# Kernel optimization log

Hardware: AMD Instinct MI355X
Metric: run time of the kernel (lower is better)

The kernel has to match this reference:

```python
import jax, jax.numpy as jnp
import numpy as np

# MSEObserver config: bit=4, symmetric=False, ch_axis=-1
QMIN, QMAX = 0, 15          # asymmetric int4: [0, 2^4 - 1]
NUM = 100                   # range-grid resolution
EPS = np.float32(np.finfo(np.float32).eps)


def setup_inputs() -> dict:
    key = jax.random.key(0)
    x_orig = jax.random.normal(key, (1024, 4096), dtype=jnp.float32)
    return {"x_orig": x_orig}


def _search_2d(x):
    # per-tensor (ch_axis == -1) 2D grid search over (range, zero_point)
    x_min = jnp.min(x)
    x_max = jnp.max(x)
    xrange = x_max - x_min
    qrange = float(QMAX - QMIN)
    zps = jnp.arange(QMIN, QMAX + 1, dtype=jnp.float32)  # [Z] candidate zp shifts

    def step(carry, i):
        best_score, best_min, best_max = carry
        tmp_max = xrange / NUM * i           # tmp_min == 0
        tmp_delta = tmp_max / qrange
        new_min = jnp.maximum(-zps * tmp_delta, x_min)           # [Z]
        new_max = jnp.minimum(tmp_max - zps * tmp_delta, x_max)  # [Z]
        # calculate_qparams (asymmetric)
        min_neg = jnp.minimum(new_min, 0.0)
        max_pos = jnp.maximum(new_max, 0.0)
        scale = jnp.maximum((max_pos - min_neg) / qrange, EPS)   # [Z]
        zp = jnp.clip(QMIN - jnp.round(min_neg / scale), QMIN, QMAX)  # [Z]
        s = scale[:, None, None]
        z = zp[:, None, None]
        # fake_quantize_per_tensor_affine, vectorized over Z candidates
        xq = (jnp.clip(jnp.round(x[None] / s) + z, QMIN, QMAX) - z) * s  # [Z,T,D]
        score = jnp.mean(jnp.square(xq - x[None]), axis=(1, 2))  # [Z], lp_loss p=2
        j = jnp.argmin(score)
        sc = score[j]
        better = sc < best_score
        best_min = jnp.where(better, new_min[j], best_min)
        best_max = jnp.where(better, new_max[j], best_max)
        best_score = jnp.minimum(best_score, sc)
        return (best_score, best_min, best_max), None

    init = (jnp.float32(1e10), x_min, x_max)
    iis = jnp.arange(1, NUM + 1, dtype=jnp.float32)
    (best_score, best_min, best_max), _ = jax.lax.scan(step, init, iis)
    return best_min, best_max


def reference(x_orig) -> jnp.ndarray:
    # randn input => one_side_dist == 'no', symmetric == False -> perform_2D_search
    x = x_orig.astype(jnp.float32)
    best_min, best_max = _search_2d(x)
    # buffer update: min_val = min(+inf, best_min), max_val = max(-inf, best_max)
    return jnp.stack([best_min, best_max])
```

## Files before the change

kernel.cpp:

```cpp
#include <hip/hip_runtime.h>
#include <math.h>

#define NUM_I 100
#define NZ    16
#define NCAND (NUM_I * NZ)
#define NBL   4096
#define G2    256
#define BLK   1024
#define SLICE 16384
#define BPT   (NBL / BLK)
#define F32_EPS 1.1920928955078125e-07f
#define AGENT __HIP_MEMORY_SCOPE_AGENT

struct WSL {
    unsigned* ctrs;
    double*   score;
    float*    pmin; float* pmax;
    float4*   params; float2* ranges; float* mm;
    double*   scoreFB;
    size_t    small_needed;
};

__host__ __device__ static inline WSL make_ws(char* w0) {
    WSL L; char* w = w0;
    L.ctrs   = (unsigned*)w; w += 64;
    L.score  = (double*)w;   w += sizeof(double) * NCAND;
    L.pmin   = (float*)w;    w += sizeof(float) * G2;
    L.pmax   = (float*)w;    w += sizeof(float) * G2;
    L.params = (float4*)w;   w += sizeof(float4) * NCAND;
    L.ranges = (float2*)w;   w += sizeof(float2) * NCAND;
    L.mm     = (float*)w;    w += sizeof(float) * 4;
    size_t head = (size_t)(w - w0);
    L.small_needed = (head + 15) & ~(size_t)15;
    L.scoreFB = L.score;
    return L;
}

static __device__ __forceinline__ float rfl_f(float v) {
    return __int_as_float(__builtin_amdgcn_readfirstlane(__float_as_int(v)));
}
static __device__ __forceinline__ double agent_load_f64(const double* p) {
    return __hip_atomic_load(p, __ATOMIC_RELAXED, AGENT);
}
static __device__ __forceinline__ int bin_loc(float v, float lo, float invw) {
    int b = (int)floorf((v - lo) * invw);
    return min(max(b, 0), NBL - 1);
}
static __device__ __forceinline__ void gbar(unsigned* ctr, int nblk) {
    __syncthreads();
    if (threadIdx.x == 0) {
        __hip_atomic_fetch_add(ctr, 1u, __ATOMIC_ACQ_REL, AGENT);
        while (__hip_atomic_load(ctr, __ATOMIC_RELAXED, AGENT) < (unsigned)nblk)
            __builtin_amdgcn_s_sleep(8);
        (void)__hip_atomic_load(ctr, __ATOMIC_ACQUIRE, AGENT);
    }
    __syncthreads();
}

__global__ __launch_bounds__(BLK, 4) void k_fused(const float* __restrict__ x, int n4,
                                                  char* wsbase, float* __restrict__ out) {
    WSL L = make_ws(wsbase);
    __shared__ __align__(16) float ssort[SLICE];
    __shared__ unsigned Cb[NBL];
    __shared__ double   S1p[NBL];
    __shared__ double   dpart[BLK];
    __shared__ unsigned upart[BLK];
    __shared__ double   stot[1];
    __shared__ float    sxm[2];
    __shared__ int      islast;
    const int tid = threadIdx.x, blk = blockIdx.x;
    const float4* x4 = (const float4*)x;
    const int per4 = (n4 + G2 - 1) / G2;
    const int beg4 = blk * per4, end4 = min(beg4 + per4, n4);
    const int len = (end4 > beg4) ? (end4 - beg4) * 4 : 0;

    {
        int gtid = blk * BLK + tid;
        if (gtid < NCAND) L.score[gtid] = 0.0;
        float* rmin = (float*)dpart; float* rmax = rmin + BLK;
        float lmin = 3.0e38f, lmax = -3.0e38f;
        for (int i = beg4 + tid; i < end4; i += BLK) {
            float4 v = x4[i];
            lmin = fminf(lmin, fminf(fminf(v.x, v.y), fminf(v.z, v.w)));
            lmax = fmaxf(lmax, fmaxf(fmaxf(v.x, v.y), fmaxf(v.z, v.w)));
        }
        rmin[tid] = lmin; rmax[tid] = lmax;
        __syncthreads();
        for (int s = BLK / 2; s > 0; s >>= 1) {
            if (tid < s) {
                rmin[tid] = fminf(rmin[tid], rmin[tid + s]);
                rmax[tid] = fmaxf(rmax[tid], rmax[tid + s]);
            }
            __syncthreads();
        }
        if (tid == 0) { L.pmin[blk] = rmin[0]; L.pmax[blk] = rmax[0]; }
    }
    gbar(&L.ctrs[0], G2);

    {
        float* rmin = (float*)dpart; float* rmax = rmin + BLK;
        float lmin = (tid < G2) ? L.pmin[tid] : 3.0e38f;
        float lmax = (tid < G2) ? L.pmax[tid] : -3.0e38f;
        rmin[tid] = lmin; rmax[tid] = lmax;
        __syncthreads();
        for (int s = BLK / 2; s > 0; s >>= 1) {
            if (tid < s) {
                rmin[tid] = fminf(rmin[tid], rmin[tid + s]);
                rmax[tid] = fmaxf(rmax[tid], rmax[tid + s]);
            }
            __syncthreads();
        }
        if (tid == 0) { sxm[0] = rmin[0]; sxm[1] = rmax[0]; }
        __syncthreads();
    }
    const float x_min = sxm[0], x_max = sxm[1];
    const float rangef = x_max - x_min;
    const float lo = x_min;
    const float invw = (rangef > 0.0f) ? ((float)NBL / rangef) : 0.0f;

    if (len > 0) {
        for (int b = tid; b < NBL; b += BLK) Cb[b] = 0u;
        __syncthreads();
        for (int i = beg4 + tid; i < end4; i += BLK) {
            float4 v = x4[i];
            atomicAdd(&Cb[bin_loc(v.x, lo, invw)], 1u);
            atomicAdd(&Cb[bin_loc(v.y, lo, invw)], 1u);
            atomicAdd(&Cb[bin_loc(v.z, lo, invw)], 1u);
            atomicAdd(&Cb[bin_loc(v.w, lo, invw)], 1u);
        }
        __syncthreads();
        unsigned cl[BPT]; unsigned ps = 0;
        #pragma unroll
        for (int k = 0; k < BPT; k++) { cl[k] = Cb[tid * BPT + k]; ps += cl[k]; }
        upart[tid] = ps;
        __syncthreads();
        for (int off = 1; off < BLK; off <<= 1) {
            unsigned v = (tid >= off) ? upart[tid - off] : 0u;
            __syncthreads();
            upart[tid] += v;
            __syncthreads();
        }
        unsigned run = upart[tid] - ps;
        #pragma unroll
        for (int k = 0; k < BPT; k++) { Cb[tid * BPT + k] = run; run += cl[k]; }
        __syncthreads();
        for (int i = beg4 + tid; i < end4; i += BLK) {
            float4 v = x4[i];
            unsigned p;
            p = atomicAdd(&Cb[bin_loc(v.x, lo, invw)], 1u); ssort[p] = v.x;
            p = atomicAdd(&Cb[bin_loc(v.y, lo, invw)], 1u); ssort[p] = v.y;
            p = atomicAdd(&Cb[bin_loc(v.z, lo, invw)], 1u); ssort[p] = v.z;
            p = atomicAdd(&Cb[bin_loc(v.w, lo, invw)], 1u); ssort[p] = v.w;
        }
        __syncthreads();
        for (int k = 0; k < BPT; k++) {
            int b = tid + k * BLK;
            unsigned st = (b == 0) ? 0u : Cb[b - 1], en = Cb[b];
            double s1 = 0.0;
            for (unsigned i = st; i < en; i++) s1 += (double)ssort[i];
            S1p[b] = s1;
        }
        __syncthreads();
        double l1[BPT];
        double a1 = 0.0;
        #pragma unroll
        for (int k = 0; k < BPT; k++) { l1[k] = S1p[tid * BPT + k]; a1 += l1[k]; }
        dpart[tid] = a1;
        __syncthreads();
        for (int off = 1; off < BLK; off <<= 1) {
            double v1 = (tid >= off) ? dpart[tid - off] : 0.0;
            __syncthreads();
            dpart[tid] += v1;
            __syncthreads();
        }
        double b1 = dpart[tid] - a1;
        #pragma unroll
        for (int k = 0; k < BPT; k++) {
            int b = tid * BPT + k;
            S1p[b] = b1; b1 += l1[k];
        }
        if (tid == BLK - 1) stot[0] = dpart[BLK - 1];
        __syncthreads();

        const double totS1 = stot[0];
        for (int q = 0; q < (NCAND + BLK - 1) / BLK; q++) {
            int cand = q * BLK + ((tid + blk) & (BLK - 1));
            if (cand >= NCAND) continue;
            int zi; double sd;
            {
#pragma clang fp contract(off)
                float step = rangef / 100.0f;
                int ii = cand >> 4, z = cand & 15;
                float fi = (float)(ii + 1);
                float tmp_max   = step * fi;
                float tmp_delta = tmp_max / 15.0f;
                float t = (float)z * tmp_delta;
                float new_min = fmaxf(-t, x_min);
                float new_max = fminf(tmp_max - t, x_max);
                float min_neg = fminf(new_min, 0.0f);
                float max_pos = fmaxf(new_max, 0.0f);
                float scale = fmaxf((max_pos - min_neg) / 15.0f, F32_EPS);
                float zp = 0.0f - rintf(min_neg / scale);
                zp = fminf(fmaxf(zp, 0.0f), 15.0f);
                zi = (int)zp; sd = (double)scale;
            }
            double prevC = 0.0, prev1 = 0.0, sc = 0.0;
            for (int j = 0; j <= 15; j++) {
                double Cc, C1;
                if (j < 15) {
                    double td = ((double)(j - zi) + 0.5) * sd;
                    float tf = (float)td;
                    int bf = bin_loc(tf, lo, invw);
                    unsigned st = (bf == 0) ? 0u : Cb[bf - 1], en = Cb[bf];
                    unsigned cnt = 0; double s1 = 0.0;
                    unsigned i = st;
                    for (; i < en && (i & 3u); i++) {
                        float v = ssort[i];
                        if (v < tf) { cnt++; s1 += (double)v; }
                    }
                    for (; i + 4u <= en; i += 4u) {
                        float4 v4 = *reinterpret_cast<const float4*>(&ssort[i]);
                        float m0 = (v4.x < tf) ? v4.x : 0.0f;
                        float m1 = (v4.y < tf) ? v4.y : 0.0f;
                        float m2 = (v4.z < tf) ? v4.z : 0.0f;
                        float m3 = (v4.w < tf) ? v4.w : 0.0f;
                        cnt += (v4.x < tf); cnt += (v4.y < tf);
                        cnt += (v4.z < tf); cnt += (v4.w < tf);
                        s1 += (double)((m0 + m1) + (m2 + m3));
                    }
                    for (; i < en; i++) {
                        float v = ssort[i];
                        if (v < tf) { cnt++; s1 += (double)v; }
                    }
                    Cc = (double)st + (double)cnt;
                    C1 = S1p[bf] + s1;
                } else {
                    Cc = (double)len; C1 = totS1;
                }
                double ms = (double)(j - zi) * sd;
                sc += ms * (ms * (Cc - prevC) - 2.0 * (C1 - prev1));
                prevC = Cc; prev1 = C1;
            }
            atomicAdd(&L.score[cand], sc);
        }
    }

    __syncthreads();
    if (tid == 0) {
        __threadfence();
        unsigned old = atomicAdd(&L.ctrs[1], 1u);
        islast = (old == gridDim.x - 1) ? 1 : 0;
    }
    __syncthreads();
    if (!islast) return;
    __threadfence();

    double* bsc = dpart;
    int*    bix = (int*)upart;
    double best = 1.0e300; int bidx = 0x7fffffff;
    for (int c = tid; c < NCAND; c += BLK) {
        double sc = agent_load_f64(&L.score[c]);
        if (sc < best) { best = sc; bidx = c; }
    }
    bsc[tid] = best; bix[tid] = bidx;
    __syncthreads();
    for (int s = BLK / 2; s > 0; s >>= 1) {
        if (tid < s) {
            double so = bsc[tid + s]; int io = bix[tid + s];
            if (so < bsc[tid] || (so == bsc[tid] && io < bix[tid])) { bsc[tid] = so; bix[tid] = io; }
        }
        __syncthreads();
    }
    if (tid == 0) {
        float bmin = x_min, bmax = x_max;
        if (bix[0] != 0x7fffffff) {
#pragma clang fp contract(off)
            int cand = bix[0];
            float step = rangef / 100.0f;
            int ii = cand >> 4, z = cand & 15;
            float fi = (float)(ii + 1);
            float tmp_max   = step * fi;
            float tmp_delta = tmp_max / 15.0f;
            float t = (float)z * tmp_delta;
            bmin = fmaxf(-t, x_min);
            bmax = fminf(tmp_max - t, x_max);
        }
        out[0] = bmin; out[1] = bmax;
    }
}

__global__ __launch_bounds__(256) void k_params_fb(const float* __restrict__ x, int n4,
                                                   float4* __restrict__ params,
                                                   float2* __restrict__ ranges,
                                                   double* __restrict__ score,
                                                   float* __restrict__ mm) {
#pragma clang fp contract(off)
    __shared__ float smin[256], smax[256];
    const float4* x4 = (const float4*)x;
    float lmin = 3.0e38f, lmax = -3.0e38f;
    for (int i = threadIdx.x; i < n4; i += 256) {
        float4 v = x4[i];
        lmin = fminf(lmin, fminf(fminf(v.x, v.y), fminf(v.z, v.w)));
        lmax = fmaxf(lmax, fmaxf(fmaxf(v.x, v.y), fmaxf(v.z, v.w)));
    }
    smin[threadIdx.x] = lmin; smax[threadIdx.x] = lmax;
    __syncthreads();
    for (int s = 128; s > 0; s >>= 1) {
        if (threadIdx.x < s) {
            smin[threadIdx.x] = fminf(smin[threadIdx.x], smin[threadIdx.x + s]);
            smax[threadIdx.x] = fmaxf(smax[threadIdx.x], smax[threadIdx.x + s]);
        }
        __syncthreads();
    }
    float x_min = smin[0], x_max = smax[0];
    if (threadIdx.x == 0) { mm[0] = x_min; mm[1] = x_max; }
    float xrange = x_max - x_min;
    float step = xrange / 100.0f;
    for (int c = threadIdx.x; c < NCAND; c += 256) {
        int ii = c >> 4;
        int z  = c & 15;
        float fi = (float)(ii + 1);
        float tmp_max   = step * fi;
        float tmp_delta = tmp_max / 15.0f;
        float t = (float)z * tmp_delta;
        float new_min = fmaxf(-t, x_min);
        float new_max = fminf(tmp_max - t, x_max);
        float min_neg = fminf(new_min, 0.0f);
        float max_pos = fmaxf(new_max, 0.0f);
        float scale = fmaxf((max_pos - min_neg) / 15.0f, F32_EPS);
        float zp = 0.0f - rintf(min_neg / scale);
        zp = fminf(fmaxf(zp, 0.0f), 15.0f);
        float inv = (float)(1.0 / (double)scale);
        params[c] = make_float4(scale, inv, 0.0f - zp, 15.0f - zp);
        ranges[c] = make_float2(new_min, new_max);
        score[c]  = 0.0;
    }
}

__global__ __launch_bounds__(256) void k_score_bf(const float* __restrict__ x, int n4,
                                                  const float4* __restrict__ params,
                                                  double* __restrict__ score) {
    const int tid = blockIdx.x * 256 + threadIdx.x;
    const int T = gridDim.x * 256;
    const float4* x4 = (const float4*)x;
    float xs[16];
    #pragma unroll
    for (int k = 0; k < 4; k++) {
        int i4 = tid + k * T;
        float4 v;
        if (i4 < n4) v = x4[i4];
        else { v.x = 0.0f; v.y = 0.0f; v.z = 0.0f; v.w = 0.0f; }
        xs[4*k+0] = v.x; xs[4*k+1] = v.y; xs[4*k+2] = v.z; xs[4*k+3] = v.w;
    }
    int c = (int)((blockIdx.x * 37u) % NCAND);
    for (int k = 0; k < NCAND; k++) {
        float4 p = params[c];
        float s   = rfl_f(p.x);
        float inv = rfl_f(p.y);
        float lo  = rfl_f(p.z);
        float hi  = rfl_f(p.w);
        float acc = 0.0f;
        #pragma unroll
        for (int e = 0; e < 16; e++) {
            float r = rintf(xs[e] * inv);
            r = fminf(fmaxf(r, lo), hi);
            float d = fmaf(r, s, -xs[e]);
            acc = fmaf(d, d, acc);
        }
        #pragma unroll
        for (int off = 32; off > 0; off >>= 1)
            acc += __shfl_xor(acc, off);
        if ((threadIdx.x & 63) == 0)
            atomicAdd(&score[c], (double)acc);
        c++; if (c >= NCAND) c -= NCAND;
    }
}

__global__ void k_final_fb(const double* __restrict__ score,
                           const float2* __restrict__ ranges,
                           const float* __restrict__ mm,
                           float* __restrict__ out) {
    if (blockIdx.x == 0 && threadIdx.x == 0) {
        double best = 1.0e300;
        float bmin = mm[0], bmax = mm[1];
        for (int c = 0; c < NCAND; c++) {
            double sc = score[c];
            if (sc < best) { best = sc; bmin = ranges[c].x; bmax = ranges[c].y; }
        }
        out[0] = bmin;
        out[1] = bmax;
    }
}

extern "C" void kernel_launch(void* const* d_in, const int* in_sizes, int n_in,
                              void* d_out, int out_size, void* d_ws, size_t ws_size,
                              hipStream_t stream) {
    const float* x = (const float*)d_in[0];
    int n  = in_sizes[0];
    int n4 = n / 4;
    float* out = (float*)d_out;
    WSL L = make_ws((char*)d_ws);

    int per4 = (n4 + G2 - 1) / G2;
    bool ok = (ws_size >= L.small_needed) && ((n % 4) == 0) && (per4 * 4 <= SLICE) && (n4 > 0);

    if (ok) {
        hipMemsetAsync(d_ws, 0, 64, stream);
        k_fused<<<G2, BLK, 0, stream>>>(x, n4, (char*)d_ws, out);
    } else if (ws_size >= L.small_needed) {
        k_params_fb<<<1, 256, 0, stream>>>(x, n4, L.params, L.ranges, L.scoreFB, L.mm);
        int blocks = ((n4 + 3) / 4 + 255) / 256;
        k_score_bf<<<blocks, 256, 0, stream>>>(x, n4, L.params, L.scoreFB);
        k_final_fb<<<1, 64, 0, stream>>>(L.scoreFB, L.ranges, L.mm, out);
    }
}
```

Baseline: 137.7 us.

## Split per-candidate threshold loop across 16 lanes with shuffle reduction

Each candidate's 15 quantization-threshold lookups are spread across a group of 16 lanes instead of being handled serially by one thread. The telescoping score sum is rewritten algebraically into independent per-threshold terms, and these are combined with xor shuffles before one lane issues the atomic add. This gives more parallelism and shorter serial loops, and only one lane in each 16-lane group does the atomic. The cost is 16x more candidate-parameter recomputation, more divergent bin scans, and a changed floating-point summation order.

New measurement: 143.7 us. 1.04x slower.

```diff
diff --git a/kernel.cpp b/kernel.cpp
--- a/kernel.cpp
+++ b/kernel.cpp
@@ -182,33 +182,33 @@
         if (tid == BLK - 1) stot[0] = dpart[BLK - 1];
         __syncthreads();
 
-        const double totS1 = stot[0];
-        for (int q = 0; q < (NCAND + BLK - 1) / BLK; q++) {
-            int cand = q * BLK + ((tid + blk) & (BLK - 1));
-            if (cand >= NCAND) continue;
-            int zi; double sd;
-            {
+        {
+            const double totS1 = stot[0];
+            const int group = tid >> 4;
+            const int l     = tid & 15;
+            for (int q = 0; q < NCAND / 64; q++) {
+                int cand = (q * 64 + group + blk) % NCAND;
+                int zi; double sd;
+                {
 #pragma clang fp contract(off)
-                float step = rangef / 100.0f;
-                int ii = cand >> 4, z = cand & 15;
-                float fi = (float)(ii + 1);
-                float tmp_max   = step * fi;
-                float tmp_delta = tmp_max / 15.0f;
-                float t = (float)z * tmp_delta;
-                float new_min = fmaxf(-t, x_min);
-                float new_max = fminf(tmp_max - t, x_max);
-                float min_neg = fminf(new_min, 0.0f);
-                float max_pos = fmaxf(new_max, 0.0f);
-                float scale = fmaxf((max_pos - min_neg) / 15.0f, F32_EPS);
-                float zp = 0.0f - rintf(min_neg / scale);
-                zp = fminf(fmaxf(zp, 0.0f), 15.0f);
-                zi = (int)zp; sd = (double)scale;
-            }
-            double prevC = 0.0, prev1 = 0.0, sc = 0.0;
-            for (int j = 0; j <= 15; j++) {
-                double Cc, C1;
-                if (j < 15) {
-                    double td = ((double)(j - zi) + 0.5) * sd;
+                    float step = rangef / 100.0f;
+                    int ii = cand >> 4, z = cand & 15;
+                    float fi = (float)(ii + 1);
+                    float tmp_max   = step * fi;
+                    float tmp_delta = tmp_max / 15.0f;
+                    float t = (float)z * tmp_delta;
+                    float new_min = fmaxf(-t, x_min);
+                    float new_max = fminf(tmp_max - t, x_max);
+                    float min_neg = fminf(new_min, 0.0f);
+                    float max_pos = fmaxf(new_max, 0.0f);
+                    float scale = fmaxf((max_pos - min_neg) / 15.0f, F32_EPS);
+                    float zp = 0.0f - rintf(min_neg / scale);
+                    zp = fminf(fmaxf(zp, 0.0f), 15.0f);
+                    zi = (int)zp; sd = (double)scale;
+                }
+                double term;
+                if (l < 15) {
+                    double td = ((double)(l - zi) + 0.5) * sd;
                     float tf = (float)td;
                     int bf = bin_loc(tf, lo, invw);
                     unsigned st = (bf == 0) ? 0u : Cb[bf - 1], en = Cb[bf];
@@ -232,16 +232,19 @@
                         float v = ssort[i];
                         if (v < tf) { cnt++; s1 += (double)v; }
                     }
-                    Cc = (double)st + (double)cnt;
-                    C1 = S1p[bf] + s1;
+                    double Cj = (double)st + (double)cnt;
+                    double Sj = S1p[bf] + s1;
+                    term = 2.0 * sd * Sj - sd * sd * (double)(2 * (l - zi) + 1) * Cj;
                 } else {
-                    Cc = (double)len; C1 = totS1;
+                    double ms15 = (double)(15 - zi) * sd;
+                    term = ms15 * ((double)len * ms15 - 2.0 * totS1);
                 }
-                double ms = (double)(j - zi) * sd;
-                sc += ms * (ms * (Cc - prevC) - 2.0 * (C1 - prev1));
-                prevC = Cc; prev1 = C1;
+                term += __shfl_xor(term, 1);
+                term += __shfl_xor(term, 2);
+                term += __shfl_xor(term, 4);
+                term += __shfl_xor(term, 8);
+                if (l == 0) atomicAdd(&L.score[cand], term);
             }
-            atomicAdd(&L.score[cand], sc);
         }
     }
 
```
